# Optimization experiments

Hardware: AMD Instinct MI355X
Metric: run time of the kernel (lower is better)

## Reference

```python
import jax, jax.numpy as jnp
import numpy as np

EMBED_DIM = 1024
NUM_HEADS = 16
HEAD_DIM = EMBED_DIM // NUM_HEADS
SEQ_LEN = 4096


def setup_inputs() -> dict:
    key = jax.random.key(0)
    kx, kq, kk, kv = jax.random.split(key, 4)
    x = jax.random.normal(kx, (SEQ_LEN, EMBED_DIM), dtype=jnp.float32)
    Wq = jax.random.normal(kq, (EMBED_DIM, EMBED_DIM), dtype=jnp.float32)
    Wk = jax.random.normal(kk, (EMBED_DIM, EMBED_DIM), dtype=jnp.float32)
    Wv = jax.random.normal(kv, (EMBED_DIM, EMBED_DIM), dtype=jnp.float32)
    return {"x": x, "Wq": Wq, "Wk": Wk, "Wv": Wv}


def reference(x, Wq, Wk, Wv):
    seq_len, embed_dim = x.shape
    h, d = NUM_HEADS, HEAD_DIM
    # project then split heads: [S, E] -> [H, S, D]
    q = (x @ Wq).reshape(seq_len, h, d).transpose(1, 0, 2)
    k = (x @ Wk).reshape(seq_len, h, d).transpose(1, 0, 2)
    v = (x @ Wv).reshape(seq_len, h, d).transpose(1, 0, 2)
    # full [H, S, S] scores, scaled by sqrt(head_dim) (faithful to original)
    scores = jnp.einsum("hsd,htd->hst", q, k) / jnp.sqrt(jnp.asarray(d, dtype=q.dtype))
    weights = jax.nn.softmax(scores, axis=-1)
    out = jnp.einsum("hst,htd->hsd", weights, v)  # [H, S, D]
    return out.transpose(1, 0, 2).reshape(seq_len, embed_dim)
```

## Files before the change

### kernel.cpp

```cpp
#include <hip/hip_runtime.h>
#include <hip/hip_bf16.h>

#define SEQ 4096
#define EMB 1024
#define NHD 16
#define HDD 64

using bf16 = __hip_bfloat16;
using bf16x8 = __attribute__((ext_vector_type(8))) short;
using f32x4  = __attribute__((ext_vector_type(4))) float;
using f32x16 = __attribute__((ext_vector_type(16))) float;
using u32x4  = __attribute__((ext_vector_type(4))) unsigned int;
using u32x2  = __attribute__((ext_vector_type(2))) unsigned int;

#define MFMA16(a, b, c) __builtin_amdgcn_mfma_f32_16x16x32_bf16((a), (b), (c), 0, 0, 0)
#define MFMA32(a, b, c) __builtin_amdgcn_mfma_f32_32x32x16_bf16((a), (b), (c), 0, 0, 0)

#define QSCALE 0.1803368801111204f

__device__ __forceinline__ float b2f(bf16 b) { return __bfloat162float(b); }

__device__ __forceinline__ void gll16(const void* g, void* l) {
    __builtin_amdgcn_global_load_lds(
        (const __attribute__((address_space(1))) unsigned int*)g,
        (__attribute__((address_space(3))) unsigned int*)l, 16, 0, 0);
}

__device__ __forceinline__ unsigned pack_bf16x2(float a, float b) {
    __hip_bfloat162 p = __float22bfloat162_rn(make_float2(a, b));
    unsigned w;
    __builtin_memcpy(&w, &p, 4);
    return w;
}

__global__ void split_kernel(const float* __restrict__ src, bf16* __restrict__ hi,
                             bf16* __restrict__ lo, int n4) {
    int i = blockIdx.x * blockDim.x + threadIdx.x;
    if (i >= n4) return;
    float4 v = ((const float4*)src)[i];
    float vv[4] = {v.x, v.y, v.z, v.w};
#pragma unroll
    for (int j = 0; j < 4; j++) {
        bf16 h = __float2bfloat16(vv[j]);
        hi[i * 4 + j] = h;
        lo[i * 4 + j] = __float2bfloat16(vv[j] - b2f(h));
    }
}

__global__ void wtrans_kernel(const float* __restrict__ Wq, const float* __restrict__ Wk,
                              const float* __restrict__ Wv,
                              bf16* __restrict__ thq, bf16* __restrict__ tlq,
                              bf16* __restrict__ thk, bf16* __restrict__ tlk,
                              bf16* __restrict__ thv, bf16* __restrict__ tlv) {
    __shared__ float tile[32][33];
    const float* W;
    bf16 *wth, *wtl;
    if (blockIdx.z == 0) { W = Wq; wth = thq; wtl = tlq; }
    else if (blockIdx.z == 1) { W = Wk; wth = thk; wtl = tlk; }
    else { W = Wv; wth = thv; wtl = tlv; }
    int n0 = blockIdx.x * 32, k0 = blockIdx.y * 32;
    int tx = threadIdx.x, ty = threadIdx.y;
    for (int r = ty; r < 32; r += 8)
        tile[r][tx] = W[(k0 + r) * EMB + n0 + tx];
    __syncthreads();
    for (int r = ty; r < 32; r += 8) {
        float v = tile[tx][r];
        bf16 h = __float2bfloat16(v);
        wth[(n0 + r) * EMB + k0 + tx] = h;
        wtl[(n0 + r) * EMB + k0 + tx] = __float2bfloat16(v - b2f(h));
    }
}

template <int NTERMS>
__device__ __forceinline__ void proj_loop(
    const bf16* __restrict__ Ah, const bf16* __restrict__ Al,
    const bf16* __restrict__ Bth, const bf16* __restrict__ Btl,
    bf16* lAh, bf16* lAl, bf16* lBh, bf16* lBl,
    int m0, int n0, int t, f32x4 (&acc)[4][4]) {
    const int wid = t >> 6, lane = t & 63, lr = lane & 15, lg = lane >> 4;
    const int wr = (wid >> 1) * 64, wc = (wid & 1) * 64;
    for (int k0 = 0; k0 < EMB; k0 += 32) {
#pragma unroll
        for (int c = t; c < 512; c += 256) {
            int row = c >> 2, slot = c & 3;
            *(uint4*)&lAh[row * 40 + slot * 8] =
                *(const uint4*)&Ah[(m0 + row) * EMB + k0 + slot * 8];
            *(uint4*)&lBh[row * 40 + slot * 8] =
                *(const uint4*)&Bth[(n0 + row) * EMB + k0 + slot * 8];
            if constexpr (NTERMS == 3) {
                *(uint4*)&lAl[row * 40 + slot * 8] =
                    *(const uint4*)&Al[(m0 + row) * EMB + k0 + slot * 8];
                *(uint4*)&lBl[row * 40 + slot * 8] =
                    *(const uint4*)&Btl[(n0 + row) * EMB + k0 + slot * 8];
            }
        }
        __syncthreads();
        bf16x8 fah[4], fbh[4], fal[4], fbl[4];
#pragma unroll
        for (int i = 0; i < 4; i++) {
            fah[i] = *(const bf16x8*)&lAh[(wr + i * 16 + lr) * 40 + lg * 8];
            fbh[i] = *(const bf16x8*)&lBh[(wc + i * 16 + lr) * 40 + lg * 8];
            if constexpr (NTERMS == 3) {
                fal[i] = *(const bf16x8*)&lAl[(wr + i * 16 + lr) * 40 + lg * 8];
                fbl[i] = *(const bf16x8*)&lBl[(wc + i * 16 + lr) * 40 + lg * 8];
            }
        }
#pragma unroll
        for (int i = 0; i < 4; i++)
#pragma unroll
            for (int j = 0; j < 4; j++) {
                acc[i][j] = MFMA16(fah[i], fbh[j], acc[i][j]);
                if constexpr (NTERMS == 3) {
                    acc[i][j] = MFMA16(fah[i], fbl[j], acc[i][j]);
                    acc[i][j] = MFMA16(fal[i], fbh[j], acc[i][j]);
                }
            }
        __syncthreads();
    }
}

__global__ __launch_bounds__(256) void proj_qkv(
    const bf16* __restrict__ xh, const bf16* __restrict__ xl,
    const bf16* __restrict__ thq, const bf16* __restrict__ tlq,
    const bf16* __restrict__ thk, const bf16* __restrict__ tlk,
    const bf16* __restrict__ thv,
    bf16* __restrict__ qh, bf16* __restrict__ ql,
    bf16* __restrict__ kh, bf16* __restrict__ kl, bf16* __restrict__ vt) {
    __shared__ __align__(16) bf16 lAh[128 * 40];
    __shared__ __align__(16) bf16 lAl[128 * 40];
    __shared__ __align__(16) bf16 lBh[128 * 40];
    __shared__ __align__(16) bf16 lBl[128 * 40];
    const int t = threadIdx.x;
    const int m0 = blockIdx.y * 128;
    const int which = blockIdx.x >> 3;
    const int n0 = (blockIdx.x & 7) * 128;

    f32x4 acc[4][4];
#pragma unroll
    for (int i = 0; i < 4; i++)
#pragma unroll
        for (int j = 0; j < 4; j++) acc[i][j] = (f32x4){0.f, 0.f, 0.f, 0.f};

    if (which == 0)
        proj_loop<3>(xh, xl, thq, tlq, lAh, lAl, lBh, lBl, m0, n0, t, acc);
    else if (which == 1)
        proj_loop<3>(xh, xl, thk, tlk, lAh, lAl, lBh, lBl, m0, n0, t, acc);
    else
        proj_loop<1>(xh, xl, thv, nullptr, lAh, lAl, lBh, lBl, m0, n0, t, acc);

    const int wid = t >> 6, lane = t & 63, lr = lane & 15, lg = lane >> 4;
    const int wr = (wid >> 1) * 64, wc = (wid & 1) * 64;

    if (which == 2) {
#pragma unroll
        for (int i = 0; i < 4; i++)
#pragma unroll
            for (int j = 0; j < 4; j++) {
                int n = n0 + wc + j * 16 + lr;
                int m = m0 + wr + i * 16 + lg * 4;
                uint2 w;
                w.x = pack_bf16x2(acc[i][j][0], acc[i][j][1]);
                w.y = pack_bf16x2(acc[i][j][2], acc[i][j][3]);
                *(uint2*)&vt[(size_t)n * SEQ + m] = w;
            }
    } else {
        float scale = (which == 0) ? QSCALE : 1.0f;
        bf16* Chi = (which == 0) ? qh : kh;
        bf16* Clo = (which == 0) ? ql : kl;
#pragma unroll
        for (int i = 0; i < 4; i++)
#pragma unroll
            for (int j = 0; j < 4; j++)
#pragma unroll
                for (int q = 0; q < 4; q++) {
                    float cv = acc[i][j][q] * scale;
                    int m = m0 + wr + i * 16 + lg * 4 + q;
                    int n = n0 + wc + j * 16 + lr;
                    bf16 hv = __float2bfloat16(cv);
                    Chi[m * EMB + n] = hv;
                    Clo[m * EMB + n] = __float2bfloat16(cv - b2f(hv));
                }
    }
}

__global__ __launch_bounds__(512, 2) void attn_kernel(
    const bf16* __restrict__ qh, const bf16* __restrict__ ql,
    const bf16* __restrict__ kh, const bf16* __restrict__ kl,
    const bf16* __restrict__ vt, float* __restrict__ out) {
    __shared__ __align__(16) bf16 lKV[2][3][64 * 64];
    const int t = threadIdx.x;
    const int swz = (blockIdx.x & 7) * 32 + (blockIdx.x >> 3);
    const int h = swz >> 4;
    const int q0 = (swz & 15) * 256;
    const int wid = t >> 6, lane = t & 63;
    const int qq = lane & 31, hi = lane >> 5;
    const int qrow = q0 + wid * 32 + qq;

    bf16x8 fqh[4], fql[4];
    {
        const bf16* qbh = qh + (size_t)qrow * EMB + h * HDD + hi * 8;
        const bf16* qbl = ql + (size_t)qrow * EMB + h * HDD + hi * 8;
#pragma unroll
        for (int ds = 0; ds < 4; ds++) {
            fqh[ds] = *(const bf16x8*)(qbh + ds * 16);
            fql[ds] = *(const bf16x8*)(qbl + ds * 16);
        }
    }

    const int srow = lane >> 3, slot = lane & 7;
    const int r = wid * 8 + srow;
    const int sb = (slot ^ (r & 7)) * 16;
    const char* gp[3];
    gp[0] = (const char*)kh + ((size_t)r * EMB + h * HDD) * 2 + sb;
    gp[1] = (const char*)kl + ((size_t)r * EMB + h * HDD) * 2 + sb;
    gp[2] = (const char*)vt + ((size_t)(h * HDD + r) * SEQ) * 2 + sb;
    bf16* lp[3];
#pragma unroll
    for (int i = 0; i < 3; i++) lp[i] = &lKV[0][i][wid * 512];

    f32x16 z16;
#pragma unroll
    for (int rg = 0; rg < 16; rg++) z16[rg] = 0.f;
    bf16x8 ONES;
    {
        short one = (short)0x3F80;
#pragma unroll
        for (int i = 0; i < 8; i++) ONES[i] = one;
    }
    f32x16 Ofr[2], Lfr;
#pragma unroll
    for (int db = 0; db < 2; db++)
#pragma unroll
        for (int rg = 0; rg < 16; rg++) Ofr[db][rg] = 0.f;
#pragma unroll
    for (int rg = 0; rg < 16; rg++) Lfr[rg] = 0.f;
    float Mr = -1e30f;

#pragma unroll
    for (int i = 0; i < 3; i++) {
        gll16(gp[i], lp[i]);
        gp[i] += (i < 2) ? (size_t)(64 * EMB * 2) : (size_t)(64 * 2);
    }
    __syncthreads();

    for (int tk = 0; tk < SEQ / 64; tk++) {
        const int cur = tk & 1;
        if (tk < SEQ / 64 - 1) {
#pragma unroll
            for (int i = 0; i < 3; i++) {
                gll16(gp[i], lp[i] + (cur ^ 1) * 12288);
                gp[i] += (i < 2) ? (size_t)(64 * EMB * 2) : (size_t)(64 * 2);
            }
        }
        const char* cKh = (const char*)&lKV[cur][0][0];
        const char* cKl = (const char*)&lKV[cur][1][0];
        const char* cV  = (const char*)&lKV[cur][2][0];

        __builtin_amdgcn_s_setprio(1);
        f32x16 sfr[2];
#pragma unroll
        for (int kb = 0; kb < 2; kb++) {
            const int row = kb * 32 + qq;
            const char* rbh = cKh + row * 128;
            const char* rbl = cKl + row * 128;
            const int sw = (row & 7) << 4;
            f32x16 a;
#pragma unroll
            for (int ds = 0; ds < 4; ds++) {
                const int off = (ds * 32 + hi * 16) ^ sw;
                bf16x8 kbh_ = *(const bf16x8*)(rbh + off);
                bf16x8 kbl_ = *(const bf16x8*)(rbl + off);
                if (ds == 0)
                    a = MFMA32(kbh_, fqh[0], z16);
                else
                    a = MFMA32(kbh_, fqh[ds], a);
                a = MFMA32(kbh_, fql[ds], a);
                a = MFMA32(kbl_, fqh[ds], a);
            }
            sfr[kb] = a;
        }
        __builtin_amdgcn_s_setprio(0);

        float m8[8];
#pragma unroll
        for (int i = 0; i < 8; i++)
            m8[i] = fmaxf(fmaxf(sfr[0][i], sfr[0][i + 8]),
                          fmaxf(sfr[1][i], sfr[1][i + 8]));
        float mx = fmaxf(fmaxf(fmaxf(m8[0], m8[1]), fmaxf(m8[2], m8[3])),
                         fmaxf(fmaxf(m8[4], m8[5]), fmaxf(m8[6], m8[7])));
        mx = fmaxf(mx, __shfl_xor(mx, 32));

        bool resc = !__all(mx <= Mr + 11.5f);
        float mn = resc ? fmaxf(Mr, mx) : Mr;
#pragma unroll
        for (int kb = 0; kb < 2; kb++)
#pragma unroll
            for (int rg = 0; rg < 16; rg++)
                sfr[kb][rg] = __builtin_exp2f(sfr[kb][rg] - mn);
        if (resc) {
            float fac = __builtin_exp2f(Mr - mn);
            Mr = mn;
#pragma unroll
            for (int db = 0; db < 2; db++)
#pragma unroll
                for (int rg = 0; rg < 16; rg++) Ofr[db][rg] *= fac;
#pragma unroll
            for (int rg = 0; rg < 16; rg++) Lfr[rg] *= fac;
        }

        bf16x8 pf[4];
#pragma unroll
        for (int sl = 0; sl < 4; sl++) {
            const int kb = sl >> 1, s8 = (sl & 1) * 8;
            unsigned w01 = pack_bf16x2(sfr[kb][s8 + 0], sfr[kb][s8 + 1]);
            unsigned w23 = pack_bf16x2(sfr[kb][s8 + 2], sfr[kb][s8 + 3]);
            unsigned w45 = pack_bf16x2(sfr[kb][s8 + 4], sfr[kb][s8 + 5]);
            unsigned w67 = pack_bf16x2(sfr[kb][s8 + 6], sfr[kb][s8 + 7]);
            u32x2 r0 = __builtin_amdgcn_permlane32_swap(w01, w45, false, false);
            u32x2 r1 = __builtin_amdgcn_permlane32_swap(w23, w67, false, false);
            u32x4 fw = {r0[0], r1[0], r0[1], r1[1]};
            bf16x8 pfv;
            __builtin_memcpy(&pfv, &fw, 16);
            pf[sl] = pfv;
        }

        __builtin_amdgcn_s_setprio(1);
#pragma unroll
        for (int sl = 0; sl < 4; sl++) {
            Lfr = MFMA32(ONES, pf[sl], Lfr);
#pragma unroll
            for (int db = 0; db < 2; db++) {
                const int vd = db * 32 + qq;
                const char* pv =
                    cV + vd * 128 + ((sl * 32 + hi * 16) ^ ((vd & 7) << 4));
                bf16x8 vf = *(const bf16x8*)pv;
                Ofr[db] = MFMA32(vf, pf[sl], Ofr[db]);
            }
        }
        __builtin_amdgcn_s_setprio(0);

        __syncthreads();
    }

    float inv = 1.0f / Lfr[0];
    float* orow = out + (size_t)qrow * EMB + h * HDD;
#pragma unroll
    for (int db = 0; db < 2; db++)
#pragma unroll
        for (int rg = 0; rg < 4; rg++) {
            float4 o = make_float4(Ofr[db][rg * 4 + 0] * inv,
                                   Ofr[db][rg * 4 + 1] * inv,
                                   Ofr[db][rg * 4 + 2] * inv,
                                   Ofr[db][rg * 4 + 3] * inv);
            *(float4*)(orow + db * 32 + rg * 8 + hi * 4) = o;
        }
}

extern "C" void kernel_launch(void* const* d_in, const int* in_sizes, int n_in,
                              void* d_out, int out_size, void* d_ws, size_t ws_size,
                              hipStream_t stream) {
    const float* x = (const float*)d_in[0];
    const float* Wq = (const float*)d_in[1];
    const float* Wk = (const float*)d_in[2];
    const float* Wv = (const float*)d_in[3];
    float* out = (float*)d_out;

    char* ws = (char*)d_ws;
    size_t off = 0;
    auto alloc = [&](size_t elems) -> bf16* {
        bf16* p = (bf16*)(ws + off);
        off += elems * sizeof(bf16);
        return p;
    };
    bf16* xh = alloc((size_t)SEQ * EMB);
    bf16* xl = alloc((size_t)SEQ * EMB);
    bf16* wthq = alloc((size_t)EMB * EMB);
    bf16* wtlq = alloc((size_t)EMB * EMB);
    bf16* wthk = alloc((size_t)EMB * EMB);
    bf16* wtlk = alloc((size_t)EMB * EMB);
    bf16* wthv = alloc((size_t)EMB * EMB);
    bf16* wtlv = alloc((size_t)EMB * EMB);
    bf16* qh = alloc((size_t)SEQ * EMB);
    bf16* ql = alloc((size_t)SEQ * EMB);
    bf16* kh = alloc((size_t)SEQ * EMB);
    bf16* kl = alloc((size_t)SEQ * EMB);
    bf16* vt = alloc((size_t)SEQ * EMB);
    (void)ws_size; (void)in_sizes; (void)n_in; (void)out_size;

    split_kernel<<<(SEQ * EMB / 4 + 255) / 256, 256, 0, stream>>>(x, xh, xl, SEQ * EMB / 4);
    wtrans_kernel<<<dim3(32, 32, 3), dim3(32, 8), 0, stream>>>(
        Wq, Wk, Wv, wthq, wtlq, wthk, wtlk, wthv, wtlv);
    proj_qkv<<<dim3(24, 32), 256, 0, stream>>>(
        xh, xl, wthq, wtlq, wthk, wtlk, wthv, qh, ql, kh, kl, vt);
    attn_kernel<<<256, 512, 0, stream>>>(qh, ql, kh, kl, vt, out);
}
```

Measured before the change: 256.8 us.

## Split attention KV range across two blocks and merge partials in combine kernel

Each (head, query-tile) attention block now handles only half of the key sequence, which doubles the grid from 256 to 512 blocks so more of the GPU's compute units are occupied. Partial outputs, running maxima and row sums go to workspace buffers reused from the x split area, and a new combine kernel rescales and merges the two halves. The row-sum MFMA against a ones vector is replaced by scalar reductions of the exponentials. The cost is an extra kernel launch plus writing and reading roughly 32 MB of fp32 partials.

```diff
diff --git a/kernel.cpp b/kernel.cpp
--- a/kernel.cpp
+++ b/kernel.cpp
@@ -186,12 +186,15 @@
 __global__ __launch_bounds__(512, 2) void attn_kernel(
     const bf16* __restrict__ qh, const bf16* __restrict__ ql,
     const bf16* __restrict__ kh, const bf16* __restrict__ kl,
-    const bf16* __restrict__ vt, float* __restrict__ out) {
+    const bf16* __restrict__ vt, float* __restrict__ pO,
+    float* __restrict__ pM, float* __restrict__ pL) {
     __shared__ __align__(16) bf16 lKV[2][3][64 * 64];
     const int t = threadIdx.x;
-    const int swz = (blockIdx.x & 7) * 32 + (blockIdx.x >> 3);
-    const int h = swz >> 4;
+    const int swz = (blockIdx.x & 7) * 64 + (blockIdx.x >> 3);
+    const int h = swz >> 5;
+    const int half = (swz >> 4) & 1;
     const int q0 = (swz & 15) * 256;
+    const int pair = h * 16 + (swz & 15);
     const int wid = t >> 6, lane = t & 63;
     const int qq = lane & 31, hi = lane >> 5;
     const int qrow = q0 + wid * 32 + qq;
@@ -210,10 +213,11 @@
     const int srow = lane >> 3, slot = lane & 7;
     const int r = wid * 8 + srow;
     const int sb = (slot ^ (r & 7)) * 16;
+    const size_t KSTEP = (size_t)64 * EMB * 2, VSTEP = 64 * 2;
     const char* gp[3];
-    gp[0] = (const char*)kh + ((size_t)r * EMB + h * HDD) * 2 + sb;
-    gp[1] = (const char*)kl + ((size_t)r * EMB + h * HDD) * 2 + sb;
-    gp[2] = (const char*)vt + ((size_t)(h * HDD + r) * SEQ) * 2 + sb;
+    gp[0] = (const char*)kh + ((size_t)r * EMB + h * HDD) * 2 + sb + half * 32 * KSTEP;
+    gp[1] = (const char*)kl + ((size_t)r * EMB + h * HDD) * 2 + sb + half * 32 * KSTEP;
+    gp[2] = (const char*)vt + ((size_t)(h * HDD + r) * SEQ) * 2 + sb + half * 32 * VSTEP;
     bf16* lp[3];
 #pragma unroll
     for (int i = 0; i < 3; i++) lp[i] = &lKV[0][i][wid * 512];
@@ -221,35 +225,27 @@
     f32x16 z16;
 #pragma unroll
     for (int rg = 0; rg < 16; rg++) z16[rg] = 0.f;
-    bf16x8 ONES;
-    {
-        short one = (short)0x3F80;
-#pragma unroll
-        for (int i = 0; i < 8; i++) ONES[i] = one;
-    }
-    f32x16 Ofr[2], Lfr;
+    f32x16 Ofr[2];
 #pragma unroll
     for (int db = 0; db < 2; db++)
 #pragma unroll
         for (int rg = 0; rg < 16; rg++) Ofr[db][rg] = 0.f;
-#pragma unroll
-    for (int rg = 0; rg < 16; rg++) Lfr[rg] = 0.f;
-    float Mr = -1e30f;
+    float Mr = -1e30f, Lr = 0.f;
 
 #pragma unroll
     for (int i = 0; i < 3; i++) {
         gll16(gp[i], lp[i]);
-        gp[i] += (i < 2) ? (size_t)(64 * EMB * 2) : (size_t)(64 * 2);
+        gp[i] += (i < 2) ? KSTEP : VSTEP;
     }
     __syncthreads();
 
-    for (int tk = 0; tk < SEQ / 64; tk++) {
+    for (int tk = 0; tk < 32; tk++) {
         const int cur = tk & 1;
-        if (tk < SEQ / 64 - 1) {
+        if (tk < 31) {
 #pragma unroll
             for (int i = 0; i < 3; i++) {
                 gll16(gp[i], lp[i] + (cur ^ 1) * 12288);
-                gp[i] += (i < 2) ? (size_t)(64 * EMB * 2) : (size_t)(64 * 2);
+                gp[i] += (i < 2) ? KSTEP : VSTEP;
             }
         }
         const char* cKh = (const char*)&lKV[cur][0][0];
@@ -297,25 +293,35 @@
 #pragma unroll
             for (int rg = 0; rg < 16; rg++)
                 sfr[kb][rg] = __builtin_exp2f(sfr[kb][rg] - mn);
+        float s16[16];
+#pragma unroll
+        for (int i = 0; i < 16; i++) s16[i] = sfr[0][i] + sfr[1][i];
+        float s8[8];
+#pragma unroll
+        for (int i = 0; i < 8; i++) s8[i] = s16[i] + s16[i + 8];
+        float ps = ((s8[0] + s8[1]) + (s8[2] + s8[3])) +
+                   ((s8[4] + s8[5]) + (s8[6] + s8[7]));
+        ps += __shfl_xor(ps, 32);
         if (resc) {
             float fac = __builtin_exp2f(Mr - mn);
             Mr = mn;
+            Lr = Lr * fac + ps;
 #pragma unroll
             for (int db = 0; db < 2; db++)
 #pragma unroll
                 for (int rg = 0; rg < 16; rg++) Ofr[db][rg] *= fac;
-#pragma unroll
-            for (int rg = 0; rg < 16; rg++) Lfr[rg] *= fac;
+        } else {
+            Lr += ps;
         }
 
         bf16x8 pf[4];
 #pragma unroll
         for (int sl = 0; sl < 4; sl++) {
-            const int kb = sl >> 1, s8 = (sl & 1) * 8;
-            unsigned w01 = pack_bf16x2(sfr[kb][s8 + 0], sfr[kb][s8 + 1]);
-            unsigned w23 = pack_bf16x2(sfr[kb][s8 + 2], sfr[kb][s8 + 3]);
-            unsigned w45 = pack_bf16x2(sfr[kb][s8 + 4], sfr[kb][s8 + 5]);
-            unsigned w67 = pack_bf16x2(sfr[kb][s8 + 6], sfr[kb][s8 + 7]);
+            const int kb = sl >> 1, s8i = (sl & 1) * 8;
+            unsigned w01 = pack_bf16x2(sfr[kb][s8i + 0], sfr[kb][s8i + 1]);
+            unsigned w23 = pack_bf16x2(sfr[kb][s8i + 2], sfr[kb][s8i + 3]);
+            unsigned w45 = pack_bf16x2(sfr[kb][s8i + 4], sfr[kb][s8i + 5]);
+            unsigned w67 = pack_bf16x2(sfr[kb][s8i + 6], sfr[kb][s8i + 7]);
             u32x2 r0 = __builtin_amdgcn_permlane32_swap(w01, w45, false, false);
             u32x2 r1 = __builtin_amdgcn_permlane32_swap(w23, w67, false, false);
             u32x4 fw = {r0[0], r1[0], r0[1], r1[1]};
@@ -327,7 +333,6 @@
         __builtin_amdgcn_s_setprio(1);
 #pragma unroll
         for (int sl = 0; sl < 4; sl++) {
-            Lfr = MFMA32(ONES, pf[sl], Lfr);
 #pragma unroll
             for (int db = 0; db < 2; db++) {
                 const int vd = db * 32 + qq;
@@ -342,18 +347,45 @@
         __syncthreads();
     }
 
-    float inv = 1.0f / Lfr[0];
-    float* orow = out + (size_t)qrow * EMB + h * HDD;
+    const size_t qloc = wid * 32 + qq;
+    float* pOb = pO + (((size_t)half * 256 + pair) * 256 + qloc) * 64;
 #pragma unroll
     for (int db = 0; db < 2; db++)
 #pragma unroll
         for (int rg = 0; rg < 4; rg++) {
-            float4 o = make_float4(Ofr[db][rg * 4 + 0] * inv,
-                                   Ofr[db][rg * 4 + 1] * inv,
-                                   Ofr[db][rg * 4 + 2] * inv,
-                                   Ofr[db][rg * 4 + 3] * inv);
-            *(float4*)(orow + db * 32 + rg * 8 + hi * 4) = o;
-        }
+            float4 o = make_float4(Ofr[db][rg * 4 + 0], Ofr[db][rg * 4 + 1],
+                                   Ofr[db][rg * 4 + 2], Ofr[db][rg * 4 + 3]);
+            *(float4*)(pOb + db * 32 + rg * 8 + hi * 4) = o;
+        }
+    if (hi == 0) {
+        size_t mi = ((size_t)half * 256 + pair) * 256 + qloc;
+        pM[mi] = Mr;
+        pL[mi] = Lr;
+    }
+}
+
+__global__ __launch_bounds__(256) void combine_kernel(
+    const float* __restrict__ pO, const float* __restrict__ pM,
+    const float* __restrict__ pL, float* __restrict__ out) {
+    const int t = blockIdx.x * 256 + threadIdx.x;
+    const int qrow = t >> 8;
+    const int col = (t & 255) * 4;
+    const int h = col >> 6, d = col & 63;
+    const int qb = qrow >> 8, qloc = qrow & 255;
+    const size_t i0 = (size_t)(h * 16 + qb) * 256 + qloc;
+    const float M0 = pM[i0], M1 = pM[65536 + i0];
+    const float L0 = pL[i0], L1 = pL[65536 + i0];
+    const float Mf = fmaxf(M0, M1);
+    const float w0 = __builtin_exp2f(M0 - Mf), w1 = __builtin_exp2f(M1 - Mf);
+    const float inv = 1.0f / (L0 * w0 + L1 * w1);
+    const float4 o0 = *(const float4*)(pO + i0 * 64 + d);
+    const float4 o1 = *(const float4*)(pO + (size_t)4194304 + i0 * 64 + d);
+    float4 o;
+    o.x = (o0.x * w0 + o1.x * w1) * inv;
+    o.y = (o0.y * w0 + o1.y * w1) * inv;
+    o.z = (o0.z * w0 + o1.z * w1) * inv;
+    o.w = (o0.w * w0 + o1.w * w1) * inv;
+    *(float4*)(out + (size_t)qrow * EMB + col) = o;
 }
 
 extern "C" void kernel_launch(void* const* d_in, const int* in_sizes, int n_in,
@@ -372,6 +404,11 @@
         off += elems * sizeof(bf16);
         return p;
     };
+    bf16* qh = alloc((size_t)SEQ * EMB);
+    bf16* ql = alloc((size_t)SEQ * EMB);
+    bf16* kh = alloc((size_t)SEQ * EMB);
+    bf16* kl = alloc((size_t)SEQ * EMB);
+    bf16* vt = alloc((size_t)SEQ * EMB);
     bf16* xh = alloc((size_t)SEQ * EMB);
     bf16* xl = alloc((size_t)SEQ * EMB);
     bf16* wthq = alloc((size_t)EMB * EMB);
@@ -380,11 +417,9 @@
     bf16* wtlk = alloc((size_t)EMB * EMB);
     bf16* wthv = alloc((size_t)EMB * EMB);
     bf16* wtlv = alloc((size_t)EMB * EMB);
-    bf16* qh = alloc((size_t)SEQ * EMB);
-    bf16* ql = alloc((size_t)SEQ * EMB);
-    bf16* kh = alloc((size_t)SEQ * EMB);
-    bf16* kl = alloc((size_t)SEQ * EMB);
-    bf16* vt = alloc((size_t)SEQ * EMB);
+    float* pO = (float*)xh;
+    float* pM = pO + (size_t)2 * 256 * 256 * 64;
+    float* pL = pM + (size_t)2 * 256 * 256;
     (void)ws_size; (void)in_sizes; (void)n_in; (void)out_size;
 
     split_kernel<<<(SEQ * EMB / 4 + 255) / 256, 256, 0, stream>>>(x, xh, xl, SEQ * EMB / 4);
@@ -392,5 +427,6 @@
         Wq, Wk, Wv, wthq, wtlq, wthk, wtlk, wthv, wtlv);
     proj_qkv<<<dim3(24, 32), 256, 0, stream>>>(
         xh, xl, wthq, wtlq, wthk, wtlk, wthv, qh, ql, kh, kl, vt);
-    attn_kernel<<<256, 512, 0, stream>>>(qh, ql, kh, kl, vt, out);
-}
+    attn_kernel<<<512, 512, 0, stream>>>(qh, ql, kh, kl, vt, pO, pM, pL);
+    combine_kernel<<<4096, 256, 0, stream>>>(pO, pM, pL, out);
+}
```

Result: slower. 267.9 us (+4.3%).
